# Kernel optimization log

Hardware: AMD Instinct MI355X
Metric: run time of the kernel (lower is better)

## Reference

```python
import jax, jax.numpy as jnp
import numpy as np
from jax import lax

# BatchNorm inference with running_mean=0, running_var=1: y = gamma*x/sqrt(1+eps) + beta
_BN_INV = 1.0 / float(np.sqrt(1.0 + 1e-5))


def _conv(x, w, b, pad):
    # x: (B,C,H,W), w: (O,C,k,k)
    y = lax.conv_general_dilated(x, w, (1, 1), [(pad, pad), (pad, pad)],
                                 dimension_numbers=('NCHW', 'OIHW', 'NCHW'))
    return y + b[None, :, None, None]


def _basic(x, w, b, g, e):
    # Conv5x5(pad=2) -> BN(inference) -> ReLU
    y = _conv(x, w, b, 2)
    y = y * (g * _BN_INV)[None, :, None, None] + e[None, :, None, None]
    return jnp.maximum(y, 0.0)


def _pool(x):
    # avg_pool2d kernel=2 stride=2
    B, C, H, W = x.shape
    return x.reshape(B, C, H // 2, 2, W // 2, 2).mean(axis=(3, 5))


def _up(x, oh, ow):
    # bilinear, align_corners=True (matches F.interpolate(..., align_corners=True))
    B, C, H, W = x.shape
    ys = jnp.linspace(0.0, H - 1.0, oh)
    xs = jnp.linspace(0.0, W - 1.0, ow)
    y0 = jnp.floor(ys).astype(jnp.int32)
    y1 = jnp.minimum(y0 + 1, H - 1)
    wy = (ys - y0)[:, None]  # (oh,1)
    x0 = jnp.floor(xs).astype(jnp.int32)
    x1 = jnp.minimum(x0 + 1, W - 1)
    wx = xs - x0  # (ow,)
    xh = x[:, :, y0, :] * (1.0 - wy) + x[:, :, y1, :] * wy  # (B,C,oh,W)
    return xh[..., x0] * (1.0 - wx) + xh[..., x1] * wx       # (B,C,oh,ow)


def setup_inputs() -> dict:
    key = jax.random.key(0)
    ks = jax.random.split(key, 16)
    chans = [(64, 3), (128, 64), (256, 128), (512, 256), (512, 512),
             (512, 1024), (256, 768), (3, 384)]
    inp = {"data": jax.random.normal(ks[0], (2, 3, 512, 512), jnp.float32)}
    for n, (o, c) in enumerate(chans, 1):
        fan = 1.0 / np.sqrt(c * 25.0)
        inp[f"w{n}"] = jax.random.normal(ks[n], (o, c, 5, 5), jnp.float32) * fan
        inp[f"b{n}"] = jnp.zeros((o,), jnp.float32)
        inp[f"g{n}"] = jnp.ones((o,), jnp.float32)
        inp[f"e{n}"] = jnp.zeros((o,), jnp.float32)
    inp["wo"] = jax.random.normal(ks[9], (3, 3, 1, 1), jnp.float32) * 0.5
    inp["bo"] = jnp.zeros((3,), jnp.float32)
    return inp


def reference(data, w1, b1, g1, e1, w2, b2, g2, e2, w3, b3, g3, e3,
              w4, b4, g4, e4, w5, b5, g5, e5, w6, b6, g6, e6,
              w7, b7, g7, e7, w8, b8, g8, e8, wo, bo):
    c1 = _basic(data, w1, b1, g1, e1)                    # (B,64,H,W)
    c2 = _basic(_pool(c1), w2, b2, g2, e2)               # (B,128,H/2,W/2)
    c3 = _basic(_pool(c2), w3, b3, g3, e3)               # (B,256,H/4,W/4)
    c4 = _basic(_pool(c3), w4, b4, g4, e4)               # (B,512,H/8,W/8)
    c5 = _basic(_pool(c4), w5, b5, g5, e5)               # (B,512,H/16,W/16)
    c6 = _basic(jnp.concatenate([c4, _up(c5, c4.shape[2], c4.shape[3])], 1),
                w6, b6, g6, e6)                          # (B,512,H/8,W/8)
    c7 = _basic(jnp.concatenate([c3, _up(c6, c3.shape[2], c3.shape[3])], 1),
                w7, b7, g7, e7)                          # (B,256,H/4,W/4)
    c8 = _basic(jnp.concatenate([c2, _up(c7, c2.shape[2], c2.shape[3])], 1),
                w8, b8, g8, e8)                          # (B,3,H/2,W/2)
    core = _conv(_up(c8, data.shape[2], data.shape[3]), wo, bo, 0)  # (B,3,H,W)
    return data * core
```

## Files before the change

kernel.cpp:

```cpp
#include <hip/hip_runtime.h>
#include <hip/hip_bf16.h>

typedef _Float16 f16x8 __attribute__((ext_vector_type(8)));
typedef _Float16 f16x4 __attribute__((ext_vector_type(4)));
typedef float f32x4 __attribute__((ext_vector_type(4)));

#define BN_S 0.99999500003749975f

__device__ inline f16x8 f16x8_zero() {
  f16x8 v = {(_Float16)0.f, (_Float16)0.f, (_Float16)0.f, (_Float16)0.f,
             (_Float16)0.f, (_Float16)0.f, (_Float16)0.f, (_Float16)0.f};
  return v;
}

__device__ __forceinline__ void load_lds16(const _Float16* g, _Float16* l) {
  __builtin_amdgcn_global_load_lds(
      (const __attribute__((address_space(1))) void*)g,
      (__attribute__((address_space(3))) void*)l, 16, 0, 0);
}

__global__ void zero_out_k(float* __restrict__ out, int n) {
  const int idx = blockIdx.x * 256 + threadIdx.x;
  if (idx < n) out[idx] = 0.f;
}

__global__ void halo_k(_Float16* __restrict__ p, int Wp, int C8, int nb, int total) {
  const int idx = blockIdx.x * 256 + threadIdx.x;
  if (idx >= total) return;
  const int b = idx / nb;
  const int r = idx - b * nb;
  const int tb = 4 * Wp * C8;
  int pix, cc;
  if (r < tb) {
    const int s = r / C8;
    cc = r - s * C8;
    pix = (s < 2 * Wp) ? s : (Wp * Wp - 4 * Wp + s);
  } else {
    const int r2 = r - tb;
    const int s = r2 / C8;
    cc = r2 - s * C8;
    const int row = 2 + (s >> 2);
    const int k = s & 3;
    const int col = (k < 2) ? k : (Wp - 4 + k);
    pix = row * Wp + col;
  }
  ((f16x8*)p)[(size_t)(b * Wp * Wp + pix) * C8 + cc] = f16x8_zero();
}

__global__ void wtrans16(const float* __restrict__ src, _Float16* __restrict__ dst,
                         const float* __restrict__ g, int O, int C, int total) {
  const int idx = blockIdx.x * 256 + threadIdx.x;
  if (idx >= total) return;
  const int OC = O * C;
  const int t = idx / OC;
  const int rem = idx - t * OC;
  const int o = rem / C;
  const int c = rem - o * C;
  dst[idx] = (_Float16)(src[(size_t)(o * C + c) * 25 + t] * g[o] * BN_S);
}

__global__ void wtrans8(const float* __restrict__ src, _Float16* __restrict__ dst,
                        const float* __restrict__ g) {
  const int idx = blockIdx.x * 256 + threadIdx.x;
  if (idx >= 28800) return;
  const int c = idx / 600;
  const int r = idx - c * 600;
  const int tap = r / 24;
  const int q = r - tap * 24;
  const int o = q >> 3, j = q & 7;
  const int cin = (c < 16) ? (c * 8 + j) : (128 + (c - 16) * 8 + j);
  dst[idx] = (_Float16)(src[((size_t)o * 384 + cin) * 25 + tap] * g[o] * BN_S);
}

template <int MF, int NF, int KS, int TAG>
__global__ __launch_bounds__(256) void conv_gemm(
    const _Float16* __restrict__ in, const _Float16* __restrict__ wt,
    const float* __restrict__ gg, const float* __restrict__ bbv,
    const float* __restrict__ ev, _Float16* __restrict__ out,
    int Cin, int Cout, int lw, int lh,
    int inS, int Wpi, int bsi, int ibase,
    int outS, int outOff, int Wpo, int bso, int obase) {
  constexpr int BM = MF * 32;
  constexpr int BN = NF * 32;
  constexpr int SUB_A = BM * 32;
  constexpr int SUB_B = BN * 32;
  __shared__ _Float16 sA[2][SUB_A * KS];
  __shared__ _Float16 sB[2][SUB_B * KS];

  const int tid = threadIdx.x;
  const int lane = tid & 63;
  const int wid = tid >> 6;
  const int wm = wid >> 1, wn = wid & 1;
  const int lr = lane >> 4, lc = lane & 15;
  const int n0 = blockIdx.x * BN;
  const int m0 = blockIdx.y * BM;
  const int H = 1 << lh, W = 1 << lw;
  const int nkb = Cin >> 5;

  const int r0 = tid >> 2;
  const int chunk = (tid & 3) ^ ((r0 >> 1) & 3);

  const _Float16* a0 = wt + (size_t)(m0 + r0) * Cin + (chunk << 3);
  const _Float16* a1 = a0 + ((size_t)Cin << 6);
  const int t0off = -2 * Wpi - 2;
  const _Float16 *b0, *b1 = nullptr;
  {
    int n = n0 + r0;
    int pix0 = (n >> (lw + lh)) * bsi + ((n >> lw) & (H - 1)) * Wpi + (n & (W - 1)) + ibase;
    b0 = in + (size_t)(pix0 + t0off) * inS + (chunk << 3);
    if constexpr (BN == 128) {
      n = n0 + r0 + 64;
      int pix1 = (n >> (lw + lh)) * bsi + ((n >> lw) & (H - 1)) * Wpi + (n & (W - 1)) + ibase;
      b1 = in + (size_t)(pix1 + t0off) * inS + (chunk << 3);
    }
  }

  const int swz = (lr ^ ((lc >> 1) & 3)) << 3;

  f32x4 acc[MF][NF];
  const f32x4 vz = {0.f, 0.f, 0.f, 0.f};
#pragma unroll
  for (int i = 0; i < MF; ++i)
#pragma unroll
    for (int j = 0; j < NF; ++j) acc[i][j] = vz;

  const int np = 25 * nkb / KS;
  int kb = 0, dx = 0;
  const size_t a_tap = (size_t)Cout * Cin - ((size_t)nkb << 5);
  const int woff = wid << 9;

  auto advance = [&]() {
    a0 += 32 * KS; b0 += 32 * KS;
    if constexpr (BM == 128) a1 += 32 * KS;
    if constexpr (BN == 128) b1 += 32 * KS;
    kb += KS;
    if (kb == nkb) {
      kb = 0;
      a0 += a_tap;
      if constexpr (BM == 128) a1 += a_tap;
      int pd;
      if (++dx == 5) { dx = 0; pd = Wpi - 4; } else pd = 1;
      const ptrdiff_t bd = (ptrdiff_t)pd * inS - ((ptrdiff_t)nkb << 5);
      b0 += bd;
      if constexpr (BN == 128) b1 += bd;
    }
  };
  auto stage = [&](int buf) {
#pragma unroll
    for (int s = 0; s < KS; ++s) {
      _Float16* sa = sA[buf] + s * SUB_A + woff;
      _Float16* sb = sB[buf] + s * SUB_B + woff;
      load_lds16(a0 + 32 * s, sa);
      if constexpr (BM == 128) load_lds16(a1 + 32 * s, sa + 2048);
      load_lds16(b0 + 32 * s, sb);
      if constexpr (BN == 128) load_lds16(b1 + 32 * s, sb + 2048);
    }
  };

  stage(0);
  __syncthreads();

  int cur = 0;
  for (int t = 0; t < np; ++t) {
    if (t + 1 < np) {
      advance();
      stage(cur ^ 1);
    }
    const _Float16* pA = sA[cur];
    const _Float16* pB = sB[cur];
#pragma unroll
    for (int s = 0; s < KS; ++s) {
      f16x8 af[MF], bf[NF];
#pragma unroll
      for (int i = 0; i < MF; ++i)
        af[i] = *(const f16x8*)(pA + s * SUB_A + ((wm * (MF * 16) + (i << 4) + lc) << 5) + swz);
#pragma unroll
      for (int i = 0; i < NF; ++i)
        bf[i] = *(const f16x8*)(pB + s * SUB_B + ((wn * (NF * 16) + (i << 4) + lc) << 5) + swz);
#pragma unroll
      for (int mi = 0; mi < MF; ++mi)
#pragma unroll
        for (int ni = 0; ni < NF; ++ni)
          acc[mi][ni] =
              __builtin_amdgcn_mfma_f32_16x16x32_f16(af[mi], bf[ni], acc[mi][ni], 0, 0, 0);
    }
    __syncthreads();
    cur ^= 1;
  }

#pragma unroll
  for (int mi = 0; mi < MF; ++mi) {
    const int ob = m0 + wm * (MF * 16) + (mi << 4) + (lr << 2);
    const f32x4 gv = *(const f32x4*)(gg + ob);
    const f32x4 bv = *(const f32x4*)(bbv + ob);
    const f32x4 evv = *(const f32x4*)(ev + ob);
#pragma unroll
    for (int ni = 0; ni < NF; ++ni) {
      const int n = n0 + wn * (NF * 16) + (ni << 4) + lc;
      const int y = (n >> lw) & (H - 1);
      const int x = n & (W - 1);
      const int bb_ = n >> (lw + lh);
      const size_t op = (size_t)(bb_ * bso + y * Wpo + x + obase) * outS + outOff + ob;
      f16x4 h;
#pragma unroll
      for (int j = 0; j < 4; ++j) {
        const float s = gv[j] * BN_S;
        float v = acc[mi][ni][j] + (bv[j] * s + evv[j]);
        v = v > 0.f ? v : 0.f;
        h[j] = (_Float16)v;
      }
      *(f16x4*)(out + op) = h;
    }
  }
}

__global__ __launch_bounds__(256) void conv1_k(
    const float* __restrict__ data, const float* __restrict__ w1,
    const float* __restrict__ g1, const float* __restrict__ b1,
    const float* __restrict__ e1, _Float16* __restrict__ out) {
  __shared__ float patch[3][20][20];
  const int tid = threadIdx.x;
  const int bid = blockIdx.x;
  const int tx = bid & 31, ty = (bid >> 5) & 31, b = bid >> 10;

  for (int i = tid; i < 1200; i += 256) {
    const int c = i / 400;
    const int r = i - c * 400;
    const int pyy = r / 20;
    const int pxx = r - pyy * 20;
    const int gy = (ty << 4) + pyy - 2, gx = (tx << 4) + pxx - 2;
    float v = 0.f;
    if ((unsigned)gy < 512u && (unsigned)gx < 512u)
      v = data[((size_t)(b * 3 + c) << 18) + (gy << 9) + gx];
    patch[c][pyy][pxx] = v;
  }
  __syncthreads();

  const int py = tid >> 4, px = tid & 15;
  float acc[64];
#pragma unroll
  for (int o = 0; o < 64; ++o) acc[o] = 0.f;

  for (int c = 0; c < 3; ++c)
    for (int dy = 0; dy < 5; ++dy) {
#pragma unroll
      for (int dx = 0; dx < 5; ++dx) {
        const float v = patch[c][py + dy][px + dx];
        const float* wb = w1 + c * 25 + dy * 5 + dx;
#pragma unroll
        for (int o = 0; o < 64; ++o) acc[o] = fmaf(v, wb[o * 75], acc[o]);
      }
    }

  const int y = (ty << 4) + py, x = (tx << 4) + px;
  _Float16* op = out + ((size_t)(((b << 9) + y) << 9) + x) * 64;
#pragma unroll
  for (int oc = 0; oc < 8; ++oc) {
    f16x8 h;
#pragma unroll
    for (int j = 0; j < 8; ++j) {
      const int o = (oc << 3) + j;
      const float s = g1[o] * BN_S;
      const float t = b1[o] * s + e1[o];
      float v = fmaf(acc[o], s, t);
      v = v > 0.f ? v : 0.f;
      h[j] = (_Float16)v;
    }
    *(f16x8*)(op + (oc << 3)) = h;
  }
}

__global__ void pool_k(const _Float16* __restrict__ in, _Float16* __restrict__ out,
                       int inS, int outS, int Wpi, int bsi, int ibase,
                       int Wpo, int bso, int obase,
                       int lwo, int lho, int lcc, int total) {
  const int idx = blockIdx.x * 256 + threadIdx.x;
  if (idx >= total) return;
  const int cc = idx & ((1 << lcc) - 1);
  const int pix = idx >> lcc;
  const int x = pix & ((1 << lwo) - 1);
  const int y = (pix >> lwo) & ((1 << lho) - 1);
  const int b = pix >> (lwo + lho);
  const int ip = b * bsi + (y << 1) * Wpi + (x << 1) + ibase;
  const _Float16* p = in + (size_t)ip * inS + (cc << 3);
  const f16x8 v00 = *(const f16x8*)p;
  const f16x8 v01 = *(const f16x8*)(p + inS);
  const f16x8 v10 = *(const f16x8*)(p + (size_t)Wpi * inS);
  const f16x8 v11 = *(const f16x8*)(p + (size_t)(Wpi + 1) * inS);
  f16x8 r;
#pragma unroll
  for (int j = 0; j < 8; ++j)
    r[j] = (_Float16)(((float)v00[j] + (float)v01[j] + (float)v10[j] + (float)v11[j]) * 0.25f);
  const int op = b * bso + y * Wpo + x + obase;
  *(f16x8*)(out + (size_t)op * outS + (cc << 3)) = r;
}

__global__ void up_k(const _Float16* __restrict__ in, _Float16* __restrict__ out,
                     int inS, int outS, int outOff,
                     int Wpi, int bsi, int ibase,
                     int Wpo, int bso, int obase,
                     int lwi, int lhi, int lcc, float scale, int total) {
  const int idx = blockIdx.x * 256 + threadIdx.x;
  if (idx >= total) return;
  const int cc = idx & ((1 << lcc) - 1);
  const int pix = idx >> lcc;
  const int lwo = lwi + 1, lho = lhi + 1;
  const int ox = pix & ((1 << lwo) - 1);
  const int oy = (pix >> lwo) & ((1 << lho) - 1);
  const int b = pix >> (lwo + lho);
  const int Hi = 1 << lhi, Wi = 1 << lwi;
  const float fy = oy * scale;
  const int y0 = (int)fy;
  const float wy = fy - y0;
  const int y1 = min(y0 + 1, Hi - 1);
  const float fx = ox * scale;
  const int x0 = (int)fx;
  const float wx = fx - x0;
  const int x1 = min(x0 + 1, Wi - 1);
  const int rbase = b * bsi + ibase;
  const _Float16* basep = in + (cc << 3);
  const f16x8 v00 = *(const f16x8*)(basep + (size_t)(rbase + y0 * Wpi + x0) * inS);
  const f16x8 v01 = *(const f16x8*)(basep + (size_t)(rbase + y0 * Wpi + x1) * inS);
  const f16x8 v10 = *(const f16x8*)(basep + (size_t)(rbase + y1 * Wpi + x0) * inS);
  const f16x8 v11 = *(const f16x8*)(basep + (size_t)(rbase + y1 * Wpi + x1) * inS);
  f16x8 r;
#pragma unroll
  for (int j = 0; j < 8; ++j) {
    const float top = (float)v00[j] * (1.f - wx) + (float)v01[j] * wx;
    const float bot = (float)v10[j] * (1.f - wx) + (float)v11[j] * wx;
    r[j] = (_Float16)(top * (1.f - wy) + bot * wy);
  }
  const int op = b * bso + oy * Wpo + ox + obase;
  *(f16x8*)(out + (size_t)op * outS + outOff + (cc << 3)) = r;
}

__global__ __launch_bounds__(256) void conv8_lds(
    const _Float16* __restrict__ inA, const _Float16* __restrict__ inB,
    const _Float16* __restrict__ wt, const float* __restrict__ b8,
    const float* __restrict__ g8, const float* __restrict__ e8,
    _Float16* __restrict__ out) {
  __shared__ f16x8 patch[2][20][20];
  const int tid = threadIdx.x;
  const int bid = blockIdx.x;
  const int tx = bid & 15, ty = (bid >> 4) & 15, b = bid >> 8;
  const int px = tid & 15, py = tid >> 4;
  const int x0 = tx << 4, y0 = ty << 4;

  float a0 = 0.f, a1 = 0.f, a2 = 0.f;
  for (int c = 0; c < 48; ++c) {
    const _Float16* sbase;
    int str;
    if (c < 16) { sbase = inA + ((size_t)b << 23) + (c << 3); str = 128; }
    else        { sbase = inB + ((size_t)b << 24) + ((c - 16) << 3); str = 256; }
    for (int i = tid; i < 400; i += 256) {
      const int pyy = i / 20, pxx = i - pyy * 20;
      const int gy = y0 + pyy - 2, gx = x0 + pxx - 2;
      f16x8 v = f16x8_zero();
      if ((unsigned)gy < 256u && (unsigned)gx < 256u)
        v = *(const f16x8*)(sbase + (size_t)((gy << 8) + gx) * str);
      patch[c & 1][pyy][pxx] = v;
    }
    __syncthreads();
    const _Float16* wb_c = wt + c * 600;
#pragma unroll
    for (int dy = 0; dy < 5; ++dy) {
#pragma unroll
      for (int dxx = 0; dxx < 5; ++dxx) {
        const f16x8 v = patch[c & 1][py + dy][px + dxx];
        const _Float16* wb = wb_c + (dy * 5 + dxx) * 24;
#pragma unroll
        for (int j = 0; j < 8; ++j) {
          const float f = (float)v[j];
          a0 = fmaf(f, (float)wb[j], a0);
          a1 = fmaf(f, (float)wb[8 + j], a1);
          a2 = fmaf(f, (float)wb[16 + j], a2);
        }
      }
    }
  }

  const float s0 = g8[0] * BN_S, t0 = b8[0] * s0 + e8[0];
  const float s1 = g8[1] * BN_S, t1 = b8[1] * s1 + e8[1];
  const float s2 = g8[2] * BN_S, t2 = b8[2] * s2 + e8[2];
  float r0 = a0 + t0, r1 = a1 + t1, r2 = a2 + t2;
  r0 = r0 > 0.f ? r0 : 0.f;
  r1 = r1 > 0.f ? r1 : 0.f;
  r2 = r2 > 0.f ? r2 : 0.f;
  f16x4 h;
  h[0] = (_Float16)r0; h[1] = (_Float16)r1; h[2] = (_Float16)r2; h[3] = (_Float16)0.f;
  const int opix = (b << 16) + ((y0 + py) << 8) + (x0 + px);
  *(f16x4*)(out + (size_t)opix * 4) = h;
}

__global__ void final_k(const float* __restrict__ data, const _Float16* __restrict__ c8,
                        const float* __restrict__ wo, const float* __restrict__ bo,
                        float* __restrict__ out) {
  const int idx = blockIdx.x * 256 + threadIdx.x;
  const int x = idx & 511, y = (idx >> 9) & 511, b = idx >> 18;
  const float sc = 255.f / 511.f;
  const float fy = y * sc;
  const int y0 = (int)fy;
  const float wy = fy - y0;
  const int y1 = min(y0 + 1, 255);
  const float fx = x * sc;
  const int x0 = (int)fx;
  const float wx = fx - x0;
  const int x1 = min(x0 + 1, 255);
  const f16x4 v00 = *(const f16x4*)(c8 + (size_t)((((b << 8) + y0) << 8) + x0) * 4);
  const f16x4 v01 = *(const f16x4*)(c8 + (size_t)((((b << 8) + y0) << 8) + x1) * 4);
  const f16x4 v10 = *(const f16x4*)(c8 + (size_t)((((b << 8) + y1) << 8) + x0) * 4);
  const f16x4 v11 = *(const f16x4*)(c8 + (size_t)((((b << 8) + y1) << 8) + x1) * 4);
  float u[3];
#pragma unroll
  for (int j = 0; j < 3; ++j) {
    const float top = (float)v00[j] * (1.f - wx) + (float)v01[j] * wx;
    const float bot = (float)v10[j] * (1.f - wx) + (float)v11[j] * wx;
    u[j] = top * (1.f - wy) + bot * wy;
  }
#pragma unroll
  for (int c = 0; c < 3; ++c) {
    const float core = bo[c] + wo[c * 3 + 0] * u[0] + wo[c * 3 + 1] * u[1] + wo[c * 3 + 2] * u[2];
    const size_t oi = ((size_t)(b * 3 + c) << 18) + (y << 9) + x;
    out[oi] = data[oi] * core;
  }
}

extern "C" void kernel_launch(void* const* d_in, const int* in_sizes, int n_in,
                              void* d_out, int out_size, void* d_ws, size_t ws_size,
                              hipStream_t stream) {
  const float* data = (const float*)d_in[0];
  const float *w[9], *bb[9], *gg[9], *ee[9];
  for (int n = 1; n <= 8; ++n) {
    w[n] = (const float*)d_in[1 + (n - 1) * 4];
    bb[n] = (const float*)d_in[2 + (n - 1) * 4];
    gg[n] = (const float*)d_in[3 + (n - 1) * 4];
    ee[n] = (const float*)d_in[4 + (n - 1) * 4];
  }
  const float* wo = (const float*)d_in[33];
  const float* bo = (const float*)d_in[34];
  float* out = (float*)d_out;
  (void)in_sizes; (void)n_in;

  const size_t NEEDED = 194810112ull;
  if (ws_size < NEEDED) {
    zero_out_k<<<(out_size + 255) / 256, 256, 0, stream>>>(out, out_size);
    return;
  }
  char* base = (char*)d_ws;
  size_t off = 0;
  auto alloc = [&](size_t bytes) -> char* {
    char* p = base + off;
    off += (bytes + 255) & ~(size_t)255;
    return p;
  };
  _Float16* W2t = (_Float16*)alloc(409600);
  _Float16* W3t = (_Float16*)alloc(1638400);
  _Float16* W4t = (_Float16*)alloc(6553600);
  _Float16* W5t = (_Float16*)alloc(13107200);
  _Float16* W6t = (_Float16*)alloc(26214400);
  _Float16* W7t = (_Float16*)alloc(9830400);
  _Float16* W8t = (_Float16*)alloc(57600);
  char* Rbig = alloc(72466432);
  char* c2b_ = alloc(33554432);
  char* R1 = alloc(17305600);
  char* R2 = alloc(13672448);

  _Float16* c1 = (_Float16*)Rbig;
  _Float16* cat7 = (_Float16*)Rbig;
  _Float16* cat6 = (_Float16*)(Rbig + 53526528);
  _Float16* up7b = (_Float16*)Rbig;
  _Float16* c2buf = (_Float16*)c2b_;
  _Float16* p1 = (_Float16*)R1;
  _Float16* c6 = (_Float16*)R1;
  _Float16* c7 = (_Float16*)R1;
  _Float16* c8 = (_Float16*)R1;
  _Float16* p2 = (_Float16*)R2;
  _Float16* p3 = (_Float16*)(R2 + 8921088);
  _Float16* p4 = (_Float16*)(R2 + 8921088);
  _Float16* c5 = (_Float16*)(R2 + 8921088 + 2654208);

  halo_k<<<(33024 + 255) / 256, 256, 0, stream>>>(p1, 260, 8, 16512, 33024);
  halo_k<<<(33280 + 255) / 256, 256, 0, stream>>>(p2, 132, 16, 16640, 33280);
  halo_k<<<(33792 + 255) / 256, 256, 0, stream>>>(p3, 68, 32, 16896, 33792);

  wtrans16<<<(25 * 128 * 64 + 255) / 256, 256, 0, stream>>>(w[2], W2t, gg[2], 128, 64, 25 * 128 * 64);
  wtrans16<<<(25 * 256 * 128 + 255) / 256, 256, 0, stream>>>(w[3], W3t, gg[3], 256, 128, 25 * 256 * 128);
  wtrans16<<<(25 * 512 * 256 + 255) / 256, 256, 0, stream>>>(w[4], W4t, gg[4], 512, 256, 25 * 512 * 256);
  wtrans16<<<(25 * 512 * 512 + 255) / 256, 256, 0, stream>>>(w[5], W5t, gg[5], 512, 512, 25 * 512 * 512);
  wtrans16<<<(25 * 512 * 1024 + 255) / 256, 256, 0, stream>>>(w[6], W6t, gg[6], 512, 1024, 25 * 512 * 1024);
  wtrans16<<<(25 * 256 * 768 + 255) / 256, 256, 0, stream>>>(w[7], W7t, gg[7], 256, 768, 25 * 256 * 768);
  wtrans8<<<(28800 + 255) / 256, 256, 0, stream>>>(w[8], W8t, gg[8]);

  conv1_k<<<2048, 256, 0, stream>>>(data, w[1], gg[1], bb[1], ee[1], c1);
  pool_k<<<1048576 / 256, 256, 0, stream>>>(c1, p1, 64, 64, 512, 262144, 0,
                                            260, 67600, 522, 8, 8, 3, 1048576);
  halo_k<<<(199680 + 255) / 256, 256, 0, stream>>>(cat7, 132, 96, 99840, 199680);
  halo_k<<<(135168 + 255) / 256, 256, 0, stream>>>(cat6, 68, 128, 67584, 135168);

  conv_gemm<4, 4, 1, 2><<<dim3(1024, 1), 256, 0, stream>>>(p1, W2t, gg[2], bb[2], ee[2], c2buf,
      64, 128, 8, 8, 64, 260, 67600, 522, 128, 0, 256, 65536, 0);
  pool_k<<<524288 / 256, 256, 0, stream>>>(c2buf, p2, 128, 128, 256, 65536, 0,
                                           132, 17424, 266, 7, 7, 4, 524288);
  conv_gemm<4, 4, 2, 3><<<dim3(256, 2), 256, 0, stream>>>(p2, W3t, gg[3], bb[3], ee[3], cat7,
      128, 256, 7, 7, 128, 132, 17424, 266, 768, 0, 132, 17424, 266);
  pool_k<<<262144 / 256, 256, 0, stream>>>(cat7, p3, 768, 256, 132, 17424, 266,
                                           68, 4624, 138, 6, 6, 5, 262144);
  conv_gemm<2, 4, 2, 4><<<dim3(64, 8), 256, 0, stream>>>(p3, W4t, gg[4], bb[4], ee[4], cat6,
      256, 512, 6, 6, 256, 68, 4624, 138, 1024, 0, 68, 4624, 138);
  halo_k<<<(34816 + 255) / 256, 256, 0, stream>>>(p4, 36, 64, 17408, 34816);
  pool_k<<<131072 / 256, 256, 0, stream>>>(cat6, p4, 1024, 512, 68, 4624, 138,
                                           36, 1296, 74, 5, 5, 6, 131072);
  conv_gemm<2, 2, 2, 5><<<dim3(32, 8), 256, 0, stream>>>(p4, W5t, gg[5], bb[5], ee[5], c5,
      512, 512, 5, 5, 512, 36, 1296, 74, 512, 0, 32, 1024, 0);
  up_k<<<524288 / 256, 256, 0, stream>>>(c5, cat6, 512, 1024, 512,
                                         32, 1024, 0, 68, 4624, 138,
                                         5, 5, 6, 31.f / 63.f, 524288);
  conv_gemm<2, 4, 2, 6><<<dim3(64, 8), 256, 0, stream>>>(cat6, W6t, gg[6], bb[6], ee[6], c6,
      1024, 512, 6, 6, 1024, 68, 4624, 138, 512, 0, 64, 4096, 0);
  up_k<<<2097152 / 256, 256, 0, stream>>>(c6, cat7, 512, 768, 256,
                                          64, 4096, 0, 132, 17424, 266,
                                          6, 6, 6, 63.f / 127.f, 2097152);
  conv_gemm<4, 4, 2, 7><<<dim3(256, 2), 256, 0, stream>>>(cat7, W7t, gg[7], bb[7], ee[7], c7,
      768, 256, 7, 7, 768, 132, 17424, 266, 256, 0, 128, 16384, 0);
  up_k<<<4194304 / 256, 256, 0, stream>>>(c7, up7b, 256, 256, 0,
                                          128, 16384, 0, 256, 65536, 0,
                                          7, 7, 5, 127.f / 255.f, 4194304);
  conv8_lds<<<512, 256, 0, stream>>>(c2buf, up7b, W8t, bb[8], gg[8], ee[8], c8);
  final_k<<<524288 / 256, 256, 0, stream>>>(data, c8, wo, bo, out);
}
```

Before: 1.798 ms.

## Split conv4/5/6 GEMMs over two tap ranges with a reduction kernel

Adds a split-K mode to the conv GEMM that divides the 25 filter taps into two ranges (13 and 12) across blockIdx.z. Each half writes fp16 partial sums to scratch, and a new reduce kernel adds them and applies bias, BN scale and ReLU. It is applied to conv4, conv5 and conv6, whose grids (512 or 256 blocks) underfill the GPU, to double the number of blocks. The cost is extra partial-sum traffic, an extra launch per layer, and fp16 rounding of the partial sums, which can reduce accuracy.

```diff
diff --git a/kernel.cpp b/kernel.cpp
--- a/kernel.cpp
+++ b/kernel.cpp
@@ -72,14 +72,15 @@
   dst[idx] = (_Float16)(src[((size_t)o * 384 + cin) * 25 + tap] * g[o] * BN_S);
 }
 
-template <int MF, int NF, int KS, int TAG>
+template <int MF, int NF, int KS, int TAG, bool SPLIT>
 __global__ __launch_bounds__(256) void conv_gemm(
     const _Float16* __restrict__ in, const _Float16* __restrict__ wt,
     const float* __restrict__ gg, const float* __restrict__ bbv,
     const float* __restrict__ ev, _Float16* __restrict__ out,
     int Cin, int Cout, int lw, int lh,
     int inS, int Wpi, int bsi, int ibase,
-    int outS, int outOff, int Wpo, int bso, int obase) {
+    int outS, int outOff, int Wpo, int bso, int obase,
+    _Float16* __restrict__ part, int partN) {
   constexpr int BM = MF * 32;
   constexpr int BN = NF * 32;
   constexpr int SUB_A = BM * 32;
@@ -97,12 +98,19 @@
   const int H = 1 << lh, W = 1 << lw;
   const int nkb = Cin >> 5;
 
+  int tap0 = 0, ntp = 25;
+  if constexpr (SPLIT) {
+    tap0 = blockIdx.z ? 13 : 0;
+    ntp = blockIdx.z ? 12 : 13;
+  }
+  const int dy0 = tap0 / 5, dx0 = tap0 - dy0 * 5;
+
   const int r0 = tid >> 2;
   const int chunk = (tid & 3) ^ ((r0 >> 1) & 3);
 
-  const _Float16* a0 = wt + (size_t)(m0 + r0) * Cin + (chunk << 3);
+  const _Float16* a0 = wt + ((size_t)tap0 * Cout + m0 + r0) * Cin + (chunk << 3);
   const _Float16* a1 = a0 + ((size_t)Cin << 6);
-  const int t0off = -2 * Wpi - 2;
+  const int t0off = (dy0 - 2) * Wpi + (dx0 - 2);
   const _Float16 *b0, *b1 = nullptr;
   {
     int n = n0 + r0;
@@ -124,8 +132,8 @@
 #pragma unroll
     for (int j = 0; j < NF; ++j) acc[i][j] = vz;
 
-  const int np = 25 * nkb / KS;
-  int kb = 0, dx = 0;
+  const int np = ntp * nkb / KS;
+  int kb = 0, dx = dx0;
   const size_t a_tap = (size_t)Cout * Cin - ((size_t)nkb << 5);
   const int woff = wid << 9;
 
@@ -188,30 +196,77 @@
     cur ^= 1;
   }
 
-#pragma unroll
-  for (int mi = 0; mi < MF; ++mi) {
-    const int ob = m0 + wm * (MF * 16) + (mi << 4) + (lr << 2);
-    const f32x4 gv = *(const f32x4*)(gg + ob);
-    const f32x4 bv = *(const f32x4*)(bbv + ob);
-    const f32x4 evv = *(const f32x4*)(ev + ob);
-#pragma unroll
-    for (int ni = 0; ni < NF; ++ni) {
-      const int n = n0 + wn * (NF * 16) + (ni << 4) + lc;
-      const int y = (n >> lw) & (H - 1);
-      const int x = n & (W - 1);
-      const int bb_ = n >> (lw + lh);
-      const size_t op = (size_t)(bb_ * bso + y * Wpo + x + obase) * outS + outOff + ob;
-      f16x4 h;
-#pragma unroll
-      for (int j = 0; j < 4; ++j) {
-        const float s = gv[j] * BN_S;
-        float v = acc[mi][ni][j] + (bv[j] * s + evv[j]);
-        v = v > 0.f ? v : 0.f;
-        h[j] = (_Float16)v;
+  if constexpr (SPLIT) {
+    _Float16* pp = part + (size_t)blockIdx.z * partN;
+#pragma unroll
+    for (int mi = 0; mi < MF; ++mi) {
+      const int ob = m0 + wm * (MF * 16) + (mi << 4) + (lr << 2);
+#pragma unroll
+      for (int ni = 0; ni < NF; ++ni) {
+        const int n = n0 + wn * (NF * 16) + (ni << 4) + lc;
+        f16x4 h;
+#pragma unroll
+        for (int j = 0; j < 4; ++j) h[j] = (_Float16)acc[mi][ni][j];
+        *(f16x4*)(pp + (size_t)n * Cout + ob) = h;
       }
-      *(f16x4*)(out + op) = h;
-    }
-  }
+    }
+  } else {
+#pragma unroll
+    for (int mi = 0; mi < MF; ++mi) {
+      const int ob = m0 + wm * (MF * 16) + (mi << 4) + (lr << 2);
+      const f32x4 gv = *(const f32x4*)(gg + ob);
+      const f32x4 bv = *(const f32x4*)(bbv + ob);
+      const f32x4 evv = *(const f32x4*)(ev + ob);
+#pragma unroll
+      for (int ni = 0; ni < NF; ++ni) {
+        const int n = n0 + wn * (NF * 16) + (ni << 4) + lc;
+        const int y = (n >> lw) & (H - 1);
+        const int x = n & (W - 1);
+        const int bb_ = n >> (lw + lh);
+        const size_t op = (size_t)(bb_ * bso + y * Wpo + x + obase) * outS + outOff + ob;
+        f16x4 h;
+#pragma unroll
+        for (int j = 0; j < 4; ++j) {
+          const float s = gv[j] * BN_S;
+          float v = acc[mi][ni][j] + (bv[j] * s + evv[j]);
+          v = v > 0.f ? v : 0.f;
+          h[j] = (_Float16)v;
+        }
+        *(f16x4*)(out + op) = h;
+      }
+    }
+  }
+}
+
+__global__ void reduce_k(const _Float16* __restrict__ part, _Float16* __restrict__ out,
+                         const float* __restrict__ g, const float* __restrict__ b,
+                         const float* __restrict__ e, int partN,
+                         int lw, int lh, int outS, int outOff,
+                         int Wpo, int bso, int obase, int total) {
+  const int idx = blockIdx.x * 256 + threadIdx.x;
+  if (idx >= total) return;
+  const int i4 = idx << 2;
+  const int n = i4 >> 9;
+  const int ob = i4 & 511;
+  const f16x4 p0 = *(const f16x4*)(part + i4);
+  const f16x4 p1 = *(const f16x4*)(part + partN + i4);
+  const f32x4 gv = *(const f32x4*)(g + ob);
+  const f32x4 bv = *(const f32x4*)(b + ob);
+  const f32x4 ev = *(const f32x4*)(e + ob);
+  const int H = 1 << lh, W = 1 << lw;
+  const int y = (n >> lw) & (H - 1);
+  const int x = n & (W - 1);
+  const int bb_ = n >> (lw + lh);
+  const size_t op = (size_t)(bb_ * bso + y * Wpo + x + obase) * outS + outOff + ob;
+  f16x4 h;
+#pragma unroll
+  for (int j = 0; j < 4; ++j) {
+    const float s = gv[j] * BN_S;
+    float v = (float)p0[j] + (float)p1[j] + (bv[j] * s + ev[j]);
+    v = v > 0.f ? v : 0.f;
+    h[j] = (_Float16)v;
+  }
+  *(f16x4*)(out + op) = h;
 }
 
 __global__ __launch_bounds__(256) void conv1_k(
@@ -471,9 +526,11 @@
   _Float16* up7b = (_Float16*)Rbig;
   _Float16* c2buf = (_Float16*)c2b_;
   _Float16* p1 = (_Float16*)R1;
+  _Float16* part4 = (_Float16*)R1;
   _Float16* c6 = (_Float16*)R1;
   _Float16* c7 = (_Float16*)R1;
   _Float16* c8 = (_Float16*)R1;
+  _Float16* part56 = (_Float16*)base;
   _Float16* p2 = (_Float16*)R2;
   _Float16* p3 = (_Float16*)(R2 + 8921088);
   _Float16* p4 = (_Float16*)(R2 + 8921088);
@@ -497,31 +554,37 @@
   halo_k<<<(199680 + 255) / 256, 256, 0, stream>>>(cat7, 132, 96, 99840, 199680);
   halo_k<<<(135168 + 255) / 256, 256, 0, stream>>>(cat6, 68, 128, 67584, 135168);
 
-  conv_gemm<4, 4, 1, 2><<<dim3(1024, 1), 256, 0, stream>>>(p1, W2t, gg[2], bb[2], ee[2], c2buf,
-      64, 128, 8, 8, 64, 260, 67600, 522, 128, 0, 256, 65536, 0);
+  conv_gemm<4, 4, 1, 2, false><<<dim3(1024, 1), 256, 0, stream>>>(p1, W2t, gg[2], bb[2], ee[2], c2buf,
+      64, 128, 8, 8, 64, 260, 67600, 522, 128, 0, 256, 65536, 0, nullptr, 0);
   pool_k<<<524288 / 256, 256, 0, stream>>>(c2buf, p2, 128, 128, 256, 65536, 0,
                                            132, 17424, 266, 7, 7, 4, 524288);
-  conv_gemm<4, 4, 2, 3><<<dim3(256, 2), 256, 0, stream>>>(p2, W3t, gg[3], bb[3], ee[3], cat7,
-      128, 256, 7, 7, 128, 132, 17424, 266, 768, 0, 132, 17424, 266);
+  conv_gemm<4, 4, 2, 3, false><<<dim3(256, 2), 256, 0, stream>>>(p2, W3t, gg[3], bb[3], ee[3], cat7,
+      128, 256, 7, 7, 128, 132, 17424, 266, 768, 0, 132, 17424, 266, nullptr, 0);
   pool_k<<<262144 / 256, 256, 0, stream>>>(cat7, p3, 768, 256, 132, 17424, 266,
                                            68, 4624, 138, 6, 6, 5, 262144);
-  conv_gemm<2, 4, 2, 4><<<dim3(64, 8), 256, 0, stream>>>(p3, W4t, gg[4], bb[4], ee[4], cat6,
-      256, 512, 6, 6, 256, 68, 4624, 138, 1024, 0, 68, 4624, 138);
+  conv_gemm<2, 4, 2, 4, true><<<dim3(64, 8, 2), 256, 0, stream>>>(p3, W4t, gg[4], bb[4], ee[4], cat6,
+      256, 512, 6, 6, 256, 68, 4624, 138, 1024, 0, 68, 4624, 138, part4, 4194304);
+  reduce_k<<<1048576 / 256, 256, 0, stream>>>(part4, cat6, gg[4], bb[4], ee[4], 4194304,
+                                              6, 6, 1024, 0, 68, 4624, 138, 1048576);
   halo_k<<<(34816 + 255) / 256, 256, 0, stream>>>(p4, 36, 64, 17408, 34816);
   pool_k<<<131072 / 256, 256, 0, stream>>>(cat6, p4, 1024, 512, 68, 4624, 138,
                                            36, 1296, 74, 5, 5, 6, 131072);
-  conv_gemm<2, 2, 2, 5><<<dim3(32, 8), 256, 0, stream>>>(p4, W5t, gg[5], bb[5], ee[5], c5,
-      512, 512, 5, 5, 512, 36, 1296, 74, 512, 0, 32, 1024, 0);
+  conv_gemm<2, 2, 2, 5, true><<<dim3(32, 8, 2), 256, 0, stream>>>(p4, W5t, gg[5], bb[5], ee[5], c5,
+      512, 512, 5, 5, 512, 36, 1296, 74, 512, 0, 32, 1024, 0, part56, 1048576);
+  reduce_k<<<262144 / 256, 256, 0, stream>>>(part56, c5, gg[5], bb[5], ee[5], 1048576,
+                                             5, 5, 512, 0, 32, 1024, 0, 262144);
   up_k<<<524288 / 256, 256, 0, stream>>>(c5, cat6, 512, 1024, 512,
                                          32, 1024, 0, 68, 4624, 138,
                                          5, 5, 6, 31.f / 63.f, 524288);
-  conv_gemm<2, 4, 2, 6><<<dim3(64, 8), 256, 0, stream>>>(cat6, W6t, gg[6], bb[6], ee[6], c6,
-      1024, 512, 6, 6, 1024, 68, 4624, 138, 512, 0, 64, 4096, 0);
+  conv_gemm<2, 4, 2, 6, true><<<dim3(64, 8, 2), 256, 0, stream>>>(cat6, W6t, gg[6], bb[6], ee[6], c6,
+      1024, 512, 6, 6, 1024, 68, 4624, 138, 512, 0, 64, 4096, 0, part56, 4194304);
+  reduce_k<<<1048576 / 256, 256, 0, stream>>>(part56, c6, gg[6], bb[6], ee[6], 4194304,
+                                              6, 6, 512, 0, 64, 4096, 0, 1048576);
   up_k<<<2097152 / 256, 256, 0, stream>>>(c6, cat7, 512, 768, 256,
                                           64, 4096, 0, 132, 17424, 266,
                                           6, 6, 6, 63.f / 127.f, 2097152);
-  conv_gemm<4, 4, 2, 7><<<dim3(256, 2), 256, 0, stream>>>(cat7, W7t, gg[7], bb[7], ee[7], c7,
-      768, 256, 7, 7, 768, 132, 17424, 266, 256, 0, 128, 16384, 0);
+  conv_gemm<4, 4, 2, 7, false><<<dim3(256, 2), 256, 0, stream>>>(cat7, W7t, gg[7], bb[7], ee[7], c7,
+      768, 256, 7, 7, 768, 132, 17424, 266, 256, 0, 128, 16384, 0, nullptr, 0);
   up_k<<<4194304 / 256, 256, 0, stream>>>(c7, up7b, 256, 256, 0,
                                           128, 16384, 0, 256, 65536, 0,
                                           7, 7, 5, 127.f / 255.f, 4194304);
```

Result: no change. 1.778 ms (-1.1%).
